# Kernel tuning notes

Hardware: AMD Instinct MI355X
Metric: run time of the kernel (lower is better)

The kernel has to match this reference:

```python
import jax, jax.numpy as jnp
import numpy as np

N = 100000   # nodes
F = 128      # input features
H = 128      # hidden = 2*output_dim
Z = 64       # output_dim
E = 1600000  # message-passing edges
EP = 200000  # pos/neg decode edges each


def setup_inputs() -> dict:
    key = jax.random.key(0)
    ks = jax.random.split(key, 6)
    x = jax.random.normal(ks[0], (N, F), dtype=jnp.float32)
    edge_index = jax.random.randint(ks[1], (2, E), 0, N, dtype=jnp.int64)
    pos_edge = jax.random.randint(ks[2], (2, EP), 0, N, dtype=jnp.int64)
    neg_edge = jax.random.randint(ks[3], (2, EP), 0, N, dtype=jnp.int64)
    W1 = jax.random.normal(ks[4], (F, H), dtype=jnp.float32) / np.float32(np.sqrt(F))
    b1 = jnp.zeros((H,), jnp.float32)
    W2 = jax.random.normal(ks[5], (H, Z), dtype=jnp.float32) / np.float32(np.sqrt(H))
    b2 = jnp.zeros((Z,), jnp.float32)
    return dict(x=x, W1=W1, b1=b1, W2=W2, b2=b2,
                edge_index=edge_index, pos_edge=pos_edge, neg_edge=neg_edge)


def _gcn_conv(x, src, dst, norm, W, b, n):
    # x' = scatter_add_dst(norm * (x @ W)[src]) + b   (GCNConv, sym-normalized, self-loops)
    h = x @ W                         # [N, out]
    msg = h[src] * norm[:, None]      # [E+N, out] gather + scale
    out = jax.ops.segment_sum(msg, dst, num_segments=n)
    return out + b


def reference(x, W1, b1, W2, b2, edge_index, pos_edge, neg_edge):
    # add self-loops (GCNConv default)
    loop = jnp.arange(N, dtype=edge_index.dtype)
    src = jnp.concatenate([edge_index[0], loop])
    dst = jnp.concatenate([edge_index[1], loop])
    # symmetric normalization deg^-1/2[src] * deg^-1/2[dst]
    deg = jax.ops.segment_sum(jnp.ones(dst.shape, x.dtype), dst, num_segments=N)
    dinv = jnp.where(deg > 0, jax.lax.rsqrt(deg), 0.0)
    norm = dinv[src] * dinv[dst]
    # encoder: GCN -> ReLU -> GCN
    h = jax.nn.relu(_gcn_conv(x, src, dst, norm, W1, b1, N))
    latent = _gcn_conv(h, src, dst, norm, W2, b2, N)
    # decoder: edge dot products on pos+neg edges
    e = jnp.concatenate([pos_edge, neg_edge], axis=-1)  # [2, 2*EP]
    logits = jnp.sum(latent[e[0]] * latent[e[1]], axis=-1)
    return logits
```

## Files before the change

### kernel.cpp

```cpp
#include <hip/hip_runtime.h>

#define N_NODES 100000
#define F_IN    128
#define H_DIM   128
#define Z_DIM   64
#define E_EDGES 1600000
#define EP_EDGES 200000

#define BSHIFT 7
#define NBUCK  ((N_NODES + 127) >> 7)
#define CHUNK  4096
#define NCHUNK ((E_EDGES + CHUNK - 1) / CHUNK)

typedef __attribute__((ext_vector_type(8))) short short8;
typedef __attribute__((ext_vector_type(4))) float f32x4;
typedef unsigned int uint;
typedef unsigned short ushort;

__device__ __forceinline__ ushort f2bf(float f) {
    uint u = __float_as_uint(f);
    u += 0x7fffu + ((u >> 16) & 1u);
    return (ushort)(u >> 16);
}
__device__ __forceinline__ float bflo(uint u) { return __uint_as_float(u << 16); }
__device__ __forceinline__ float bfhi(uint u) { return __uint_as_float(u & 0xffff0000u); }


__global__ __launch_bounds__(256) void wprep_kernel(const float* __restrict__ W1,
                                                    const float* __restrict__ W2,
                                                    ushort* __restrict__ W1T,
                                                    ushort* __restrict__ W2T,
                                                    int* __restrict__ gcur) {
    int i = blockIdx.x * 256 + threadIdx.x;
    if (i < 1024) gcur[i] = 0;
    if (i < 128 * 128) {
        int n = i >> 7, k = i & 127;
        W1T[i] = f2bf(W1[k * 128 + n]);
    }
    int j = i - 128 * 128;
    if (j >= 0 && j < 64 * 128) {
        int n = j >> 7, k = j & 127;
        W2T[j] = f2bf(W2[k * 64 + n]);
    }
}


__global__ __launch_bounds__(256) void bhist_kernel(const int* __restrict__ dst,
                                                    int* __restrict__ gcur,
                                                    int* __restrict__ tbl) {
    __shared__ int lh[NBUCK];
    for (int i = threadIdx.x; i < NBUCK; i += 256) lh[i] = 0;
    __syncthreads();
    int base = blockIdx.x * CHUNK;
    int end = min(base + CHUNK, E_EDGES);
    for (int e = base + threadIdx.x; e < end; e += 256)
        atomicAdd(&lh[dst[e] >> BSHIFT], 1);
    __syncthreads();
    int* trow = tbl + (size_t)blockIdx.x * NBUCK;
    for (int i = threadIdx.x; i < NBUCK; i += 256) {
        int c = lh[i];
        trow[i] = c;
        if (c) atomicAdd(&gcur[i], c);
    }
}


__global__ __launch_bounds__(1024) void bscan_kernel(int* __restrict__ gc) {
    __shared__ int s[1024];
    int t = threadIdx.x;
    int v = (t < NBUCK) ? gc[t] : 0;
    s[t] = v;
    __syncthreads();
    #pragma unroll
    for (int off = 1; off < 1024; off <<= 1) {
        int x = (t >= off) ? s[t - off] : 0;
        __syncthreads();
        s[t] += x;
        __syncthreads();
    }
    if (t < NBUCK) gc[t] = s[t] - v;
}


__global__ __launch_bounds__(512) void chunk_scan_kernel(int* __restrict__ tbl,
                                                         const int* __restrict__ gcur) {
    __shared__ int s[512];
    int b = blockIdx.x, t = threadIdx.x;
    int v = (t < NCHUNK) ? tbl[(size_t)t * NBUCK + b] : 0;
    s[t] = v;
    __syncthreads();
    #pragma unroll
    for (int off = 1; off < 512; off <<= 1) {
        int x = (t >= off) ? s[t - off] : 0;
        __syncthreads();
        s[t] += x;
        __syncthreads();
    }
    if (t < NCHUNK)
        tbl[(size_t)t * NBUCK + b] = gcur[b] + (s[t] - v);
}


__global__ __launch_bounds__(256) void bscatter_kernel(const int* __restrict__ src,
                                                       const int* __restrict__ dst,
                                                       const int* __restrict__ tbl,
                                                       int* __restrict__ sorted) {
    __shared__ int lbase[NBUCK];
    int c = blockIdx.x;
    const int* trow = tbl + (size_t)c * NBUCK;
    for (int i = threadIdx.x; i < NBUCK; i += 256) lbase[i] = trow[i];
    __syncthreads();
    int base = c * CHUNK;
    int end = min(base + CHUNK, E_EDGES);
    for (int e = base + threadIdx.x; e < end; e += 256) {
        int d = dst[e];
        int p = atomicAdd(&lbase[d >> BSHIFT], 1);
        sorted[p] = (src[e] << 7) | (d & 127);
    }
}


__global__ __launch_bounds__(256) void bucket_csr_kernel(const int* __restrict__ sorted,
                                                         const int* __restrict__ gcur,
                                                         int* __restrict__ csr,
                                                         int* __restrict__ ends,
                                                         float* __restrict__ dinv) {
    __shared__ int lcnt[4][128], lcur[4][128];
    int b = blockIdx.x, t = threadIdx.x;
    int wave = t >> 6;
    int bstart = gcur[b];
    int bend = (b + 1 < NBUCK) ? gcur[b + 1] : E_EDGES;
    if (t < 128) { lcnt[0][t] = 0; lcnt[1][t] = 0; }
    else { int u = t - 128; lcnt[2][u] = 0; lcnt[3][u] = 0; }
    __syncthreads();
    for (int i = bstart + t; i < bend; i += 256)
        atomicAdd(&lcnt[wave][sorted[i] & 127], 1);
    __syncthreads();
    if (t < 64) {
        int w0a = lcnt[0][t], w1a = lcnt[1][t], w2a = lcnt[2][t], w3a = lcnt[3][t];
        int w0b = lcnt[0][t + 64], w1b = lcnt[1][t + 64], w2b = lcnt[2][t + 64], w3b = lcnt[3][t + 64];
        int c0 = w0a + w1a + w2a + w3a;
        int c1 = w0b + w1b + w2b + w3b;
        int s0 = c0;
        #pragma unroll
        for (int d = 1; d < 64; d <<= 1) {
            int x = __shfl_up(s0, d, 64);
            if (t >= d) s0 += x;
        }
        int tot0 = __shfl(s0, 63, 64);
        int s1 = c1;
        #pragma unroll
        for (int d = 1; d < 64; d <<= 1) {
            int x = __shfl_up(s1, d, 64);
            if (t >= d) s1 += x;
        }
        s1 += tot0;
        int basea = bstart + s0 - c0;
        int baseb = bstart + s1 - c1;
        lcur[0][t] = basea;
        lcur[1][t] = basea + w0a;
        lcur[2][t] = basea + w0a + w1a;
        lcur[3][t] = basea + w0a + w1a + w2a;
        lcur[0][t + 64] = baseb;
        lcur[1][t + 64] = baseb + w0b;
        lcur[2][t + 64] = baseb + w0b + w1b;
        lcur[3][t + 64] = baseb + w0b + w1b + w2b;
        int n0 = b * 128 + t, n1 = n0 + 64;
        if (n0 < N_NODES) { ends[n0] = bstart + s0; dinv[n0] = rsqrtf(1.0f + (float)c0); }
        if (n1 < N_NODES) { ends[n1] = bstart + s1; dinv[n1] = rsqrtf(1.0f + (float)c1); }
    }
    __syncthreads();
    for (int i = bstart + t; i < bend; i += 256) {
        int v = sorted[i];
        int p = atomicAdd(&lcur[wave][v & 127], 1);
        csr[p] = v >> 7;
    }
}


template<int NC, bool A_F32>
__global__ __launch_bounds__(256) void gemm_mfma_kernel(const void* __restrict__ Ap,
                                                        const ushort* __restrict__ BT,
                                                        const float* __restrict__ dinv,
                                                        ushort* __restrict__ C, int M) {
    constexpr int NT = NC / 16;
    __shared__ ushort Bs[4 * NT * 64 * 8];

    for (int idx = threadIdx.x; idx < 4 * NT * 64; idx += 256) {
        int l   = idx & 63;
        int nt  = (idx >> 6) % NT;
        int kc  = idx / (64 * NT);
        int m16 = l & 15, quad = l >> 4;
        ((short8*)Bs)[idx] =
            *(const short8*)(BT + ((nt * 16 + m16) * 128 + kc * 32 + quad * 8));
    }
    __syncthreads();

    int wave = threadIdx.x >> 6, lane = threadIdx.x & 63;
    int m16 = lane & 15, quad = lane >> 4;
    int row0 = (blockIdx.x * 4 + wave) * 16;
    if (row0 >= M) return;
    int arow = row0 + m16;
    if (arow >= M) arow = M - 1;

    f32x4 acc[NT];
    #pragma unroll
    for (int t = 0; t < NT; ++t) acc[t] = (f32x4){0.f, 0.f, 0.f, 0.f};

    #pragma unroll
    for (int kc = 0; kc < 4; ++kc) {
        short8 a;
        if (A_F32) {
            const float* A = (const float*)Ap;
            const float4* p = (const float4*)(A + (size_t)arow * 128 + kc * 32 + quad * 8);
            float4 x0 = p[0], x1 = p[1];
            a[0] = (short)f2bf(x0.x); a[1] = (short)f2bf(x0.y);
            a[2] = (short)f2bf(x0.z); a[3] = (short)f2bf(x0.w);
            a[4] = (short)f2bf(x1.x); a[5] = (short)f2bf(x1.y);
            a[6] = (short)f2bf(x1.z); a[7] = (short)f2bf(x1.w);
        } else {
            a = *(const short8*)((const ushort*)Ap + (size_t)arow * 128 + kc * 32 + quad * 8);
        }
        #pragma unroll
        for (int nt = 0; nt < NT; ++nt) {
            short8 b = ((const short8*)Bs)[(kc * NT + nt) * 64 + lane];
            acc[nt] = __builtin_amdgcn_mfma_f32_16x16x32_bf16(a, b, acc[nt], 0, 0, 0);
        }
    }

    #pragma unroll
    for (int r = 0; r < 4; ++r) {
        int row = row0 + quad * 4 + r;
        if (row < M) {
            float dr = dinv[row];
            #pragma unroll
            for (int nt = 0; nt < NT; ++nt)
                C[(size_t)row * NC + nt * 16 + m16] = f2bf(acc[nt][r] * dr);
        }
    }
}


__global__ __launch_bounds__(256) void gather128_kernel(const ushort* __restrict__ feat,
                                                        const float* __restrict__ bias,
                                                        const float* __restrict__ dinv,
                                                        const int* __restrict__ ends,
                                                        const int* __restrict__ csr,
                                                        ushort* __restrict__ out) {
    int wave = threadIdx.x >> 6, lane = threadIdx.x & 63;
    int half = lane >> 5, sl = lane & 31;
    int n = blockIdx.x * 4 + wave;
    const uint2* fu = (const uint2*)feat;

    float a0 = 0.f, a1 = 0.f, a2 = 0.f, a3 = 0.f;
    if (half == 0) {
        uint2 s = fu[(size_t)n * 32 + sl];
        a0 = bflo(s.x); a1 = bfhi(s.x); a2 = bflo(s.y); a3 = bfhi(s.y);
    }
    int j0 = n ? ends[n - 1] : 0, j1 = ends[n];
    int j = j0 + half;
    for (; j + 14 < j1; j += 16) {
        int s0 = csr[j],      s1 = csr[j + 2],  s2 = csr[j + 4],  s3 = csr[j + 6];
        int s4 = csr[j + 8],  s5 = csr[j + 10], s6 = csr[j + 12], s7 = csr[j + 14];
        uint2 f0 = fu[(size_t)s0 * 32 + sl];
        uint2 f1 = fu[(size_t)s1 * 32 + sl];
        uint2 f2 = fu[(size_t)s2 * 32 + sl];
        uint2 f3 = fu[(size_t)s3 * 32 + sl];
        uint2 f4 = fu[(size_t)s4 * 32 + sl];
        uint2 f5 = fu[(size_t)s5 * 32 + sl];
        uint2 f6 = fu[(size_t)s6 * 32 + sl];
        uint2 f7 = fu[(size_t)s7 * 32 + sl];
        a0 += bflo(f0.x) + bflo(f1.x) + bflo(f2.x) + bflo(f3.x)
            + bflo(f4.x) + bflo(f5.x) + bflo(f6.x) + bflo(f7.x);
        a1 += bfhi(f0.x) + bfhi(f1.x) + bfhi(f2.x) + bfhi(f3.x)
            + bfhi(f4.x) + bfhi(f5.x) + bfhi(f6.x) + bfhi(f7.x);
        a2 += bflo(f0.y) + bflo(f1.y) + bflo(f2.y) + bflo(f3.y)
            + bflo(f4.y) + bflo(f5.y) + bflo(f6.y) + bflo(f7.y);
        a3 += bfhi(f0.y) + bfhi(f1.y) + bfhi(f2.y) + bfhi(f3.y)
            + bfhi(f4.y) + bfhi(f5.y) + bfhi(f6.y) + bfhi(f7.y);
    }
    for (; j + 6 < j1; j += 8) {
        int s0 = csr[j], s1 = csr[j + 2], s2 = csr[j + 4], s3 = csr[j + 6];
        uint2 f0 = fu[(size_t)s0 * 32 + sl];
        uint2 f1 = fu[(size_t)s1 * 32 + sl];
        uint2 f2 = fu[(size_t)s2 * 32 + sl];
        uint2 f3 = fu[(size_t)s3 * 32 + sl];
        a0 += bflo(f0.x) + bflo(f1.x) + bflo(f2.x) + bflo(f3.x);
        a1 += bfhi(f0.x) + bfhi(f1.x) + bfhi(f2.x) + bfhi(f3.x);
        a2 += bflo(f0.y) + bflo(f1.y) + bflo(f2.y) + bflo(f3.y);
        a3 += bfhi(f0.y) + bfhi(f1.y) + bfhi(f2.y) + bfhi(f3.y);
    }
    for (; j < j1; j += 2) {
        uint2 f = fu[(size_t)csr[j] * 32 + sl];
        a0 += bflo(f.x); a1 += bfhi(f.x); a2 += bflo(f.y); a3 += bfhi(f.y);
    }
    a0 += __shfl_xor(a0, 32, 64);
    a1 += __shfl_xor(a1, 32, 64);
    a2 += __shfl_xor(a2, 32, 64);
    a3 += __shfl_xor(a3, 32, 64);
    if (half == 0) {
        float dn = dinv[n];
        float r0 = fmaxf(bias[sl * 4 + 0] + dn * a0, 0.f);
        float r1 = fmaxf(bias[sl * 4 + 1] + dn * a1, 0.f);
        float r2 = fmaxf(bias[sl * 4 + 2] + dn * a2, 0.f);
        float r3 = fmaxf(bias[sl * 4 + 3] + dn * a3, 0.f);
        uint2 o;
        o.x = (uint)f2bf(r0) | ((uint)f2bf(r1) << 16);
        o.y = (uint)f2bf(r2) | ((uint)f2bf(r3) << 16);
        ((uint2*)out)[(size_t)n * 32 + sl] = o;
    }
}


__global__ __launch_bounds__(256) void gather64_kernel(const ushort* __restrict__ feat,
                                                       const float* __restrict__ bias,
                                                       const float* __restrict__ dinv,
                                                       const int* __restrict__ ends,
                                                       const int* __restrict__ csr,
                                                       ushort* __restrict__ outB) {
    int wave = threadIdx.x >> 6, lane = threadIdx.x & 63;
    int half = lane >> 5, sl = lane & 31;
    int n = blockIdx.x * 4 + wave;
    const uint* fu = (const uint*)feat;

    float a0 = 0.f, a1 = 0.f;
    if (half == 0) {
        uint s = fu[(size_t)n * 32 + sl];
        a0 = bflo(s); a1 = bfhi(s);
    }
    int j0 = n ? ends[n - 1] : 0, j1 = ends[n];
    int j = j0 + half;
    for (; j + 14 < j1; j += 16) {
        int s0 = csr[j],      s1 = csr[j + 2],  s2 = csr[j + 4],  s3 = csr[j + 6];
        int s4 = csr[j + 8],  s5 = csr[j + 10], s6 = csr[j + 12], s7 = csr[j + 14];
        uint f0 = fu[(size_t)s0 * 32 + sl];
        uint f1 = fu[(size_t)s1 * 32 + sl];
        uint f2 = fu[(size_t)s2 * 32 + sl];
        uint f3 = fu[(size_t)s3 * 32 + sl];
        uint f4 = fu[(size_t)s4 * 32 + sl];
        uint f5 = fu[(size_t)s5 * 32 + sl];
        uint f6 = fu[(size_t)s6 * 32 + sl];
        uint f7 = fu[(size_t)s7 * 32 + sl];
        a0 += bflo(f0) + bflo(f1) + bflo(f2) + bflo(f3)
            + bflo(f4) + bflo(f5) + bflo(f6) + bflo(f7);
        a1 += bfhi(f0) + bfhi(f1) + bfhi(f2) + bfhi(f3)
            + bfhi(f4) + bfhi(f5) + bfhi(f6) + bfhi(f7);
    }
    for (; j + 6 < j1; j += 8) {
        int s0 = csr[j], s1 = csr[j + 2], s2 = csr[j + 4], s3 = csr[j + 6];
        uint f0 = fu[(size_t)s0 * 32 + sl];
        uint f1 = fu[(size_t)s1 * 32 + sl];
        uint f2 = fu[(size_t)s2 * 32 + sl];
        uint f3 = fu[(size_t)s3 * 32 + sl];
        a0 += bflo(f0) + bflo(f1) + bflo(f2) + bflo(f3);
        a1 += bfhi(f0) + bfhi(f1) + bfhi(f2) + bfhi(f3);
    }
    for (; j < j1; j += 2) {
        uint f = fu[(size_t)csr[j] * 32 + sl];
        a0 += bflo(f); a1 += bfhi(f);
    }
    a0 += __shfl_xor(a0, 32, 64);
    a1 += __shfl_xor(a1, 32, 64);
    if (half == 0) {
        float dn = dinv[n];
        float o0 = bias[sl * 2]     + dn * a0;
        float o1 = bias[sl * 2 + 1] + dn * a1;
        ((uint*)outB)[(size_t)n * 32 + sl] = (uint)f2bf(o0) | ((uint)f2bf(o1) << 16);
    }
}


__global__ __launch_bounds__(256) void decode_kernel(const ushort* __restrict__ latentB,
                                                     const int* __restrict__ pos,
                                                     const int* __restrict__ neg,
                                                     float* __restrict__ out) {
    int gwave = (blockIdx.x * 256 + threadIdx.x) >> 6;
    int lane = threadIdx.x & 63;
    int half = lane >> 5, sl = lane & 31;
    const uint* L = (const uint*)latentB;
    int e0 = gwave * 8 + half * 4;
    if (e0 >= 2 * EP_EDGES) return;

    int ia[4], ib[4];
    #pragma unroll
    for (int u = 0; u < 4; ++u) {
        int edge = e0 + u;
        if (edge < EP_EDGES) {
            ia[u] = pos[edge];
            ib[u] = pos[EP_EDGES + edge];
        } else {
            int e2 = edge - EP_EDGES;
            ia[u] = neg[e2];
            ib[u] = neg[EP_EDGES + e2];
        }
    }
    uint la[4], lb[4];
    #pragma unroll
    for (int u = 0; u < 4; ++u) {
        la[u] = L[(size_t)ia[u] * 32 + sl];
        lb[u] = L[(size_t)ib[u] * 32 + sl];
    }
    float v[4];
    #pragma unroll
    for (int u = 0; u < 4; ++u)
        v[u] = bflo(la[u]) * bflo(lb[u]) + bfhi(la[u]) * bfhi(lb[u]);
    #pragma unroll
    for (int u = 0; u < 4; ++u) {
        float s = v[u];
        #pragma unroll
        for (int off = 16; off > 0; off >>= 1) s += __shfl_down(s, off, 64);
        if (sl == 0) out[e0 + u] = s;
    }
}


extern "C" void kernel_launch(void* const* d_in, const int* in_sizes, int n_in,
                              void* d_out, int out_size, void* d_ws, size_t ws_size,
                              hipStream_t stream) {
    const float* x  = (const float*)d_in[0];
    const float* W1 = (const float*)d_in[1];
    const float* b1 = (const float*)d_in[2];
    const float* W2 = (const float*)d_in[3];
    const float* b2 = (const float*)d_in[4];
    const int* edge_index = (const int*)d_in[5];
    const int* pos = (const int*)d_in[6];
    const int* neg = (const int*)d_in[7];
    float* out = (float*)d_out;

    const int* src = edge_index;
    const int* dst = edge_index + E_EDGES;

    float*  dinv   = (float*)d_ws;
    int*    ends   = (int*)(dinv + N_NODES);
    int*    gcur   = ends + N_NODES;
    int*    tbl    = gcur + 1024;
    int*    sorted = tbl + NCHUNK * NBUCK;
    int*    csr    = sorted + E_EDGES;
    ushort* W1T    = (ushort*)(csr + E_EDGES);
    ushort* W2T    = W1T + 128 * 128;
    ushort* bufH   = (ushort*)(((uintptr_t)(W2T + 64 * 128) + 255) & ~(uintptr_t)255);
    ushort* bufR   = bufH + (size_t)N_NODES * 128;

    wprep_kernel<<<96, 256, 0, stream>>>(W1, W2, W1T, W2T, gcur);

    bhist_kernel<<<NCHUNK, 256, 0, stream>>>(dst, gcur, tbl);
    bscan_kernel<<<1, 1024, 0, stream>>>(gcur);
    chunk_scan_kernel<<<NBUCK, 512, 0, stream>>>(tbl, gcur);
    bscatter_kernel<<<NCHUNK, 256, 0, stream>>>(src, dst, tbl, sorted);
    bucket_csr_kernel<<<NBUCK, 256, 0, stream>>>(sorted, gcur, csr, ends, dinv);

    const int GEMM_GRID = (N_NODES + 63) / 64;

    gemm_mfma_kernel<128, true><<<GEMM_GRID, 256, 0, stream>>>(x, W1T, dinv, bufH, N_NODES);

    gather128_kernel<<<N_NODES / 4, 256, 0, stream>>>(bufH, b1, dinv, ends, csr, bufR);

    gemm_mfma_kernel<64, false><<<GEMM_GRID, 256, 0, stream>>>(bufR, W2T, dinv, bufH, N_NODES);

    ushort* latentB = bufR;
    gather64_kernel<<<N_NODES / 4, 256, 0, stream>>>(bufH, b2, dinv, ends, csr, latentB);

    decode_kernel<<<(2 * EP_EDGES) / 32, 256, 0, stream>>>(latentB, pos, neg, out);
}
```

Measured before the change: 318.7 us.

## Restructure CSR gather kernels with 16-byte loads and shuffled index broadcast

Both SpMM gather kernels now split each wave into 4 (128-dim) or 8 (64-dim) lane groups. Each lane issues 16-byte feature loads, and each group handles a different neighbor. Neighbor indices are loaded once per 64-edge batch with a coalesced read and broadcast through wave shuffles, instead of each lane re-reading csr. This aims to raise memory-level parallelism and cut index-load traffic, at the cost of more cross-lane reductions and masked tail handling. Launch bounds also request 8 blocks per CU.

```diff
diff --git a/kernel.cpp b/kernel.cpp
--- a/kernel.cpp
+++ b/kernel.cpp
@@ -241,131 +241,184 @@
 }
 
 
-__global__ __launch_bounds__(256) void gather128_kernel(const ushort* __restrict__ feat,
-                                                        const float* __restrict__ bias,
-                                                        const float* __restrict__ dinv,
-                                                        const int* __restrict__ ends,
-                                                        const int* __restrict__ csr,
-                                                        ushort* __restrict__ out) {
+__global__ __launch_bounds__(256, 8) void gather128_kernel(const ushort* __restrict__ feat,
+                                                           const float* __restrict__ bias,
+                                                           const float* __restrict__ dinv,
+                                                           const int* __restrict__ ends,
+                                                           const int* __restrict__ csr,
+                                                           ushort* __restrict__ out) {
     int wave = threadIdx.x >> 6, lane = threadIdx.x & 63;
-    int half = lane >> 5, sl = lane & 31;
+    int q = lane >> 4, ql = lane & 15;
     int n = blockIdx.x * 4 + wave;
-    const uint2* fu = (const uint2*)feat;
+    const uint4* F = (const uint4*)feat;
 
     float a0 = 0.f, a1 = 0.f, a2 = 0.f, a3 = 0.f;
-    if (half == 0) {
-        uint2 s = fu[(size_t)n * 32 + sl];
+    float a4 = 0.f, a5 = 0.f, a6 = 0.f, a7 = 0.f;
+    if (q == 0) {
+        uint4 s = F[(uint)n * 16u + (uint)ql];
         a0 = bflo(s.x); a1 = bfhi(s.x); a2 = bflo(s.y); a3 = bfhi(s.y);
+        a4 = bflo(s.z); a5 = bfhi(s.z); a6 = bflo(s.w); a7 = bfhi(s.w);
     }
     int j0 = n ? ends[n - 1] : 0, j1 = ends[n];
-    int j = j0 + half;
-    for (; j + 14 < j1; j += 16) {
-        int s0 = csr[j],      s1 = csr[j + 2],  s2 = csr[j + 4],  s3 = csr[j + 6];
-        int s4 = csr[j + 8],  s5 = csr[j + 10], s6 = csr[j + 12], s7 = csr[j + 14];
-        uint2 f0 = fu[(size_t)s0 * 32 + sl];
-        uint2 f1 = fu[(size_t)s1 * 32 + sl];
-        uint2 f2 = fu[(size_t)s2 * 32 + sl];
-        uint2 f3 = fu[(size_t)s3 * 32 + sl];
-        uint2 f4 = fu[(size_t)s4 * 32 + sl];
-        uint2 f5 = fu[(size_t)s5 * 32 + sl];
-        uint2 f6 = fu[(size_t)s6 * 32 + sl];
-        uint2 f7 = fu[(size_t)s7 * 32 + sl];
-        a0 += bflo(f0.x) + bflo(f1.x) + bflo(f2.x) + bflo(f3.x)
-            + bflo(f4.x) + bflo(f5.x) + bflo(f6.x) + bflo(f7.x);
-        a1 += bfhi(f0.x) + bfhi(f1.x) + bfhi(f2.x) + bfhi(f3.x)
-            + bfhi(f4.x) + bfhi(f5.x) + bfhi(f6.x) + bfhi(f7.x);
-        a2 += bflo(f0.y) + bflo(f1.y) + bflo(f2.y) + bflo(f3.y)
-            + bflo(f4.y) + bflo(f5.y) + bflo(f6.y) + bflo(f7.y);
-        a3 += bfhi(f0.y) + bfhi(f1.y) + bfhi(f2.y) + bfhi(f3.y)
-            + bfhi(f4.y) + bfhi(f5.y) + bfhi(f6.y) + bfhi(f7.y);
-    }
-    for (; j + 6 < j1; j += 8) {
-        int s0 = csr[j], s1 = csr[j + 2], s2 = csr[j + 4], s3 = csr[j + 6];
-        uint2 f0 = fu[(size_t)s0 * 32 + sl];
-        uint2 f1 = fu[(size_t)s1 * 32 + sl];
-        uint2 f2 = fu[(size_t)s2 * 32 + sl];
-        uint2 f3 = fu[(size_t)s3 * 32 + sl];
-        a0 += bflo(f0.x) + bflo(f1.x) + bflo(f2.x) + bflo(f3.x);
-        a1 += bfhi(f0.x) + bfhi(f1.x) + bfhi(f2.x) + bfhi(f3.x);
-        a2 += bflo(f0.y) + bflo(f1.y) + bflo(f2.y) + bflo(f3.y);
-        a3 += bfhi(f0.y) + bfhi(f1.y) + bfhi(f2.y) + bfhi(f3.y);
-    }
-    for (; j < j1; j += 2) {
-        uint2 f = fu[(size_t)csr[j] * 32 + sl];
-        a0 += bflo(f.x); a1 += bfhi(f.x); a2 += bflo(f.y); a3 += bfhi(f.y);
-    }
-    a0 += __shfl_xor(a0, 32, 64);
-    a1 += __shfl_xor(a1, 32, 64);
-    a2 += __shfl_xor(a2, 32, 64);
-    a3 += __shfl_xor(a3, 32, 64);
-    if (half == 0) {
+    for (int base = j0; base < j1; base += 64) {
+        int m = min(64, j1 - base);
+        int idxv = csr[base + min(lane, m - 1)];
+        int nch = m >> 4;
+        for (int c = 0; c < nch; ++c) {
+            int e = c * 16 + q;
+            int s0 = __shfl(idxv, e, 64);
+            int s1 = __shfl(idxv, e + 4, 64);
+            int s2 = __shfl(idxv, e + 8, 64);
+            int s3 = __shfl(idxv, e + 12, 64);
+            uint4 r0 = F[(uint)s0 * 16u + (uint)ql];
+            uint4 r1 = F[(uint)s1 * 16u + (uint)ql];
+            uint4 r2 = F[(uint)s2 * 16u + (uint)ql];
+            uint4 r3 = F[(uint)s3 * 16u + (uint)ql];
+            a0 += bflo(r0.x) + bflo(r1.x) + bflo(r2.x) + bflo(r3.x);
+            a1 += bfhi(r0.x) + bfhi(r1.x) + bfhi(r2.x) + bfhi(r3.x);
+            a2 += bflo(r0.y) + bflo(r1.y) + bflo(r2.y) + bflo(r3.y);
+            a3 += bfhi(r0.y) + bfhi(r1.y) + bfhi(r2.y) + bfhi(r3.y);
+            a4 += bflo(r0.z) + bflo(r1.z) + bflo(r2.z) + bflo(r3.z);
+            a5 += bfhi(r0.z) + bfhi(r1.z) + bfhi(r2.z) + bfhi(r3.z);
+            a6 += bflo(r0.w) + bflo(r1.w) + bflo(r2.w) + bflo(r3.w);
+            a7 += bfhi(r0.w) + bfhi(r1.w) + bfhi(r2.w) + bfhi(r3.w);
+        }
+        if (nch * 16 < m) {
+            int e = nch * 16 + q;
+            int mc = m - 1;
+            int t0 = __shfl(idxv, min(e,      mc), 64);
+            int t1 = __shfl(idxv, min(e + 4,  mc), 64);
+            int t2 = __shfl(idxv, min(e + 8,  mc), 64);
+            int t3 = __shfl(idxv, min(e + 12, mc), 64);
+            uint4 r0 = F[(uint)t0 * 16u + (uint)ql];
+            uint4 r1 = F[(uint)t1 * 16u + (uint)ql];
+            uint4 r2 = F[(uint)t2 * 16u + (uint)ql];
+            uint4 r3 = F[(uint)t3 * 16u + (uint)ql];
+            if (e < m) {
+                a0 += bflo(r0.x); a1 += bfhi(r0.x); a2 += bflo(r0.y); a3 += bfhi(r0.y);
+                a4 += bflo(r0.z); a5 += bfhi(r0.z); a6 += bflo(r0.w); a7 += bfhi(r0.w);
+            }
+            if (e + 4 < m) {
+                a0 += bflo(r1.x); a1 += bfhi(r1.x); a2 += bflo(r1.y); a3 += bfhi(r1.y);
+                a4 += bflo(r1.z); a5 += bfhi(r1.z); a6 += bflo(r1.w); a7 += bfhi(r1.w);
+            }
+            if (e + 8 < m) {
+                a0 += bflo(r2.x); a1 += bfhi(r2.x); a2 += bflo(r2.y); a3 += bfhi(r2.y);
+                a4 += bflo(r2.z); a5 += bfhi(r2.z); a6 += bflo(r2.w); a7 += bfhi(r2.w);
+            }
+            if (e + 12 < m) {
+                a0 += bflo(r3.x); a1 += bfhi(r3.x); a2 += bflo(r3.y); a3 += bfhi(r3.y);
+                a4 += bflo(r3.z); a5 += bfhi(r3.z); a6 += bflo(r3.w); a7 += bfhi(r3.w);
+            }
+        }
+    }
+    a0 += __shfl_xor(a0, 16, 64); a0 += __shfl_xor(a0, 32, 64);
+    a1 += __shfl_xor(a1, 16, 64); a1 += __shfl_xor(a1, 32, 64);
+    a2 += __shfl_xor(a2, 16, 64); a2 += __shfl_xor(a2, 32, 64);
+    a3 += __shfl_xor(a3, 16, 64); a3 += __shfl_xor(a3, 32, 64);
+    a4 += __shfl_xor(a4, 16, 64); a4 += __shfl_xor(a4, 32, 64);
+    a5 += __shfl_xor(a5, 16, 64); a5 += __shfl_xor(a5, 32, 64);
+    a6 += __shfl_xor(a6, 16, 64); a6 += __shfl_xor(a6, 32, 64);
+    a7 += __shfl_xor(a7, 16, 64); a7 += __shfl_xor(a7, 32, 64);
+    if (q == 0) {
         float dn = dinv[n];
-        float r0 = fmaxf(bias[sl * 4 + 0] + dn * a0, 0.f);
-        float r1 = fmaxf(bias[sl * 4 + 1] + dn * a1, 0.f);
-        float r2 = fmaxf(bias[sl * 4 + 2] + dn * a2, 0.f);
-        float r3 = fmaxf(bias[sl * 4 + 3] + dn * a3, 0.f);
-        uint2 o;
+        const float4* bp = (const float4*)(bias + ql * 8);
+        float4 b0 = bp[0], b1v = bp[1];
+        float r0 = fmaxf(b0.x + dn * a0, 0.f);
+        float r1 = fmaxf(b0.y + dn * a1, 0.f);
+        float r2 = fmaxf(b0.z + dn * a2, 0.f);
+        float r3 = fmaxf(b0.w + dn * a3, 0.f);
+        float r4 = fmaxf(b1v.x + dn * a4, 0.f);
+        float r5 = fmaxf(b1v.y + dn * a5, 0.f);
+        float r6 = fmaxf(b1v.z + dn * a6, 0.f);
+        float r7 = fmaxf(b1v.w + dn * a7, 0.f);
+        uint4 o;
         o.x = (uint)f2bf(r0) | ((uint)f2bf(r1) << 16);
         o.y = (uint)f2bf(r2) | ((uint)f2bf(r3) << 16);
-        ((uint2*)out)[(size_t)n * 32 + sl] = o;
-    }
-}
-
-
-__global__ __launch_bounds__(256) void gather64_kernel(const ushort* __restrict__ feat,
-                                                       const float* __restrict__ bias,
-                                                       const float* __restrict__ dinv,
-                                                       const int* __restrict__ ends,
-                                                       const int* __restrict__ csr,
-                                                       ushort* __restrict__ outB) {
+        o.z = (uint)f2bf(r4) | ((uint)f2bf(r5) << 16);
+        o.w = (uint)f2bf(r6) | ((uint)f2bf(r7) << 16);
+        ((uint4*)out)[(uint)n * 16u + (uint)ql] = o;
+    }
+}
+
+
+__global__ __launch_bounds__(256, 8) void gather64_kernel(const ushort* __restrict__ feat,
+                                                          const float* __restrict__ bias,
+                                                          const float* __restrict__ dinv,
+                                                          const int* __restrict__ ends,
+                                                          const int* __restrict__ csr,
+                                                          ushort* __restrict__ outB) {
     int wave = threadIdx.x >> 6, lane = threadIdx.x & 63;
-    int half = lane >> 5, sl = lane & 31;
+    int g = lane >> 3, gl = lane & 7;
     int n = blockIdx.x * 4 + wave;
-    const uint* fu = (const uint*)feat;
-
-    float a0 = 0.f, a1 = 0.f;
-    if (half == 0) {
-        uint s = fu[(size_t)n * 32 + sl];
-        a0 = bflo(s); a1 = bfhi(s);
+    const uint4* F = (const uint4*)feat;
+
+    float a0 = 0.f, a1 = 0.f, a2 = 0.f, a3 = 0.f;
+    float a4 = 0.f, a5 = 0.f, a6 = 0.f, a7 = 0.f;
+    if (g == 0) {
+        uint4 s = F[(uint)n * 8u + (uint)gl];
+        a0 = bflo(s.x); a1 = bfhi(s.x); a2 = bflo(s.y); a3 = bfhi(s.y);
+        a4 = bflo(s.z); a5 = bfhi(s.z); a6 = bflo(s.w); a7 = bfhi(s.w);
     }
     int j0 = n ? ends[n - 1] : 0, j1 = ends[n];
-    int j = j0 + half;
-    for (; j + 14 < j1; j += 16) {
-        int s0 = csr[j],      s1 = csr[j + 2],  s2 = csr[j + 4],  s3 = csr[j + 6];
-        int s4 = csr[j + 8],  s5 = csr[j + 10], s6 = csr[j + 12], s7 = csr[j + 14];
-        uint f0 = fu[(size_t)s0 * 32 + sl];
-        uint f1 = fu[(size_t)s1 * 32 + sl];
-        uint f2 = fu[(size_t)s2 * 32 + sl];
-        uint f3 = fu[(size_t)s3 * 32 + sl];
-        uint f4 = fu[(size_t)s4 * 32 + sl];
-        uint f5 = fu[(size_t)s5 * 32 + sl];
-        uint f6 = fu[(size_t)s6 * 32 + sl];
-        uint f7 = fu[(size_t)s7 * 32 + sl];
-        a0 += bflo(f0) + bflo(f1) + bflo(f2) + bflo(f3)
-            + bflo(f4) + bflo(f5) + bflo(f6) + bflo(f7);
-        a1 += bfhi(f0) + bfhi(f1) + bfhi(f2) + bfhi(f3)
-            + bfhi(f4) + bfhi(f5) + bfhi(f6) + bfhi(f7);
-    }
-    for (; j + 6 < j1; j += 8) {
-        int s0 = csr[j], s1 = csr[j + 2], s2 = csr[j + 4], s3 = csr[j + 6];
-        uint f0 = fu[(size_t)s0 * 32 + sl];
-        uint f1 = fu[(size_t)s1 * 32 + sl];
-        uint f2 = fu[(size_t)s2 * 32 + sl];
-        uint f3 = fu[(size_t)s3 * 32 + sl];
-        a0 += bflo(f0) + bflo(f1) + bflo(f2) + bflo(f3);
-        a1 += bfhi(f0) + bfhi(f1) + bfhi(f2) + bfhi(f3);
-    }
-    for (; j < j1; j += 2) {
-        uint f = fu[(size_t)csr[j] * 32 + sl];
-        a0 += bflo(f); a1 += bfhi(f);
-    }
-    a0 += __shfl_xor(a0, 32, 64);
-    a1 += __shfl_xor(a1, 32, 64);
-    if (half == 0) {
+    for (int base = j0; base < j1; base += 64) {
+        int m = min(64, j1 - base);
+        int idxv = csr[base + min(lane, m - 1)];
+        int nch = m >> 4;
+        for (int c = 0; c < nch; ++c) {
+            int e = c * 16 + g;
+            int s0 = __shfl(idxv, e, 64);
+            int s1 = __shfl(idxv, e + 8, 64);
+            uint4 r0 = F[(uint)s0 * 8u + (uint)gl];
+            uint4 r1 = F[(uint)s1 * 8u + (uint)gl];
+            a0 += bflo(r0.x) + bflo(r1.x); a1 += bfhi(r0.x) + bfhi(r1.x);
+            a2 += bflo(r0.y) + bflo(r1.y); a3 += bfhi(r0.y) + bfhi(r1.y);
+            a4 += bflo(r0.z) + bflo(r1.z); a5 += bfhi(r0.z) + bfhi(r1.z);
+            a6 += bflo(r0.w) + bflo(r1.w); a7 += bfhi(r0.w) + bfhi(r1.w);
+        }
+        if (nch * 16 < m) {
+            int e = nch * 16 + g;
+            int mc = m - 1;
+            int t0 = __shfl(idxv, min(e,     mc), 64);
+            int t1 = __shfl(idxv, min(e + 8, mc), 64);
+            uint4 r0 = F[(uint)t0 * 8u + (uint)gl];
+            uint4 r1 = F[(uint)t1 * 8u + (uint)gl];
+            if (e < m) {
+                a0 += bflo(r0.x); a1 += bfhi(r0.x); a2 += bflo(r0.y); a3 += bfhi(r0.y);
+                a4 += bflo(r0.z); a5 += bfhi(r0.z); a6 += bflo(r0.w); a7 += bfhi(r0.w);
+            }
+            if (e + 8 < m) {
+                a0 += bflo(r1.x); a1 += bfhi(r1.x); a2 += bflo(r1.y); a3 += bfhi(r1.y);
+                a4 += bflo(r1.z); a5 += bfhi(r1.z); a6 += bflo(r1.w); a7 += bfhi(r1.w);
+            }
+        }
+    }
+    a0 += __shfl_xor(a0, 8, 64); a0 += __shfl_xor(a0, 16, 64); a0 += __shfl_xor(a0, 32, 64);
+    a1 += __shfl_xor(a1, 8, 64); a1 += __shfl_xor(a1, 16, 64); a1 += __shfl_xor(a1, 32, 64);
+    a2 += __shfl_xor(a2, 8, 64); a2 += __shfl_xor(a2, 16, 64); a2 += __shfl_xor(a2, 32, 64);
+    a3 += __shfl_xor(a3, 8, 64); a3 += __shfl_xor(a3, 16, 64); a3 += __shfl_xor(a3, 32, 64);
+    a4 += __shfl_xor(a4, 8, 64); a4 += __shfl_xor(a4, 16, 64); a4 += __shfl_xor(a4, 32, 64);
+    a5 += __shfl_xor(a5, 8, 64); a5 += __shfl_xor(a5, 16, 64); a5 += __shfl_xor(a5, 32, 64);
+    a6 += __shfl_xor(a6, 8, 64); a6 += __shfl_xor(a6, 16, 64); a6 += __shfl_xor(a6, 32, 64);
+    a7 += __shfl_xor(a7, 8, 64); a7 += __shfl_xor(a7, 16, 64); a7 += __shfl_xor(a7, 32, 64);
+    if (g == 0) {
         float dn = dinv[n];
-        float o0 = bias[sl * 2]     + dn * a0;
-        float o1 = bias[sl * 2 + 1] + dn * a1;
-        ((uint*)outB)[(size_t)n * 32 + sl] = (uint)f2bf(o0) | ((uint)f2bf(o1) << 16);
+        const float4* bp = (const float4*)(bias + gl * 8);
+        float4 b0 = bp[0], b1v = bp[1];
+        float r0 = b0.x + dn * a0;
+        float r1 = b0.y + dn * a1;
+        float r2 = b0.z + dn * a2;
+        float r3 = b0.w + dn * a3;
+        float r4 = b1v.x + dn * a4;
+        float r5 = b1v.y + dn * a5;
+        float r6 = b1v.z + dn * a6;
+        float r7 = b1v.w + dn * a7;
+        uint4 o;
+        o.x = (uint)f2bf(r0) | ((uint)f2bf(r1) << 16);
+        o.y = (uint)f2bf(r2) | ((uint)f2bf(r3) << 16);
+        o.z = (uint)f2bf(r4) | ((uint)f2bf(r5) << 16);
+        o.w = (uint)f2bf(r6) | ((uint)f2bf(r7) << 16);
+        ((uint4*)outB)[(uint)n * 8u + (uint)gl] = o;
     }
 }
 
```

New measurement: 312.2 us. -2.1%, faster.

## Restructure CSR gathers as full-wave rows with readlane-broadcast neighbour indices

Applied to the files above, without the earlier changes.

Both aggregation kernels now use the whole 64-lane wave for one destination row instead of two half-waves that each handle alternate edges. Neighbour indices are loaded coalesced, 64 per chunk, and broadcast with readlane, so the per-edge feature addresses are wave-uniform and the scattered scalar index loads go away. Two accumulators split the dependency chain, and launch_bounds gets an occupancy hint of 8. In exchange each feature load is narrower (4 or 2 bytes per lane), so fewer bytes are in flight per instruction, which could hurt latency hiding on the random gathers.

```diff
diff --git a/kernel.cpp b/kernel.cpp
--- a/kernel.cpp
+++ b/kernel.cpp
@@ -241,132 +241,121 @@
 }
 
 
-__global__ __launch_bounds__(256) void gather128_kernel(const ushort* __restrict__ feat,
-                                                        const float* __restrict__ bias,
-                                                        const float* __restrict__ dinv,
-                                                        const int* __restrict__ ends,
-                                                        const int* __restrict__ csr,
-                                                        ushort* __restrict__ out) {
+__global__ __launch_bounds__(256, 8) void gather128_kernel(const ushort* __restrict__ feat,
+                                                           const float* __restrict__ bias,
+                                                           const float* __restrict__ dinv,
+                                                           const int* __restrict__ ends,
+                                                           const int* __restrict__ csr,
+                                                           ushort* __restrict__ out) {
     int wave = threadIdx.x >> 6, lane = threadIdx.x & 63;
-    int half = lane >> 5, sl = lane & 31;
     int n = blockIdx.x * 4 + wave;
-    const uint2* fu = (const uint2*)feat;
-
-    float a0 = 0.f, a1 = 0.f, a2 = 0.f, a3 = 0.f;
-    if (half == 0) {
-        uint2 s = fu[(size_t)n * 32 + sl];
-        a0 = bflo(s.x); a1 = bfhi(s.x); a2 = bflo(s.y); a3 = bfhi(s.y);
-    }
+    const uint* F = (const uint*)feat;
+    uint rowoff = (uint)n * 64u + (uint)lane;
+
+    uint su = F[rowoff];
+    float l0 = bflo(su), h0 = bfhi(su);
+    float l1 = 0.f, h1 = 0.f;
+
     int j0 = n ? ends[n - 1] : 0, j1 = ends[n];
-    int j = j0 + half;
-    for (; j + 14 < j1; j += 16) {
-        int s0 = csr[j],      s1 = csr[j + 2],  s2 = csr[j + 4],  s3 = csr[j + 6];
-        int s4 = csr[j + 8],  s5 = csr[j + 10], s6 = csr[j + 12], s7 = csr[j + 14];
-        uint2 f0 = fu[(size_t)s0 * 32 + sl];
-        uint2 f1 = fu[(size_t)s1 * 32 + sl];
-        uint2 f2 = fu[(size_t)s2 * 32 + sl];
-        uint2 f3 = fu[(size_t)s3 * 32 + sl];
-        uint2 f4 = fu[(size_t)s4 * 32 + sl];
-        uint2 f5 = fu[(size_t)s5 * 32 + sl];
-        uint2 f6 = fu[(size_t)s6 * 32 + sl];
-        uint2 f7 = fu[(size_t)s7 * 32 + sl];
-        a0 += bflo(f0.x) + bflo(f1.x) + bflo(f2.x) + bflo(f3.x)
-            + bflo(f4.x) + bflo(f5.x) + bflo(f6.x) + bflo(f7.x);
-        a1 += bfhi(f0.x) + bfhi(f1.x) + bfhi(f2.x) + bfhi(f3.x)
-            + bfhi(f4.x) + bfhi(f5.x) + bfhi(f6.x) + bfhi(f7.x);
-        a2 += bflo(f0.y) + bflo(f1.y) + bflo(f2.y) + bflo(f3.y)
-            + bflo(f4.y) + bflo(f5.y) + bflo(f6.y) + bflo(f7.y);
-        a3 += bfhi(f0.y) + bfhi(f1.y) + bfhi(f2.y) + bfhi(f3.y)
-            + bfhi(f4.y) + bfhi(f5.y) + bfhi(f6.y) + bfhi(f7.y);
-    }
-    for (; j + 6 < j1; j += 8) {
-        int s0 = csr[j], s1 = csr[j + 2], s2 = csr[j + 4], s3 = csr[j + 6];
-        uint2 f0 = fu[(size_t)s0 * 32 + sl];
-        uint2 f1 = fu[(size_t)s1 * 32 + sl];
-        uint2 f2 = fu[(size_t)s2 * 32 + sl];
-        uint2 f3 = fu[(size_t)s3 * 32 + sl];
-        a0 += bflo(f0.x) + bflo(f1.x) + bflo(f2.x) + bflo(f3.x);
-        a1 += bfhi(f0.x) + bfhi(f1.x) + bfhi(f2.x) + bfhi(f3.x);
-        a2 += bflo(f0.y) + bflo(f1.y) + bflo(f2.y) + bflo(f3.y);
-        a3 += bfhi(f0.y) + bfhi(f1.y) + bfhi(f2.y) + bfhi(f3.y);
-    }
-    for (; j < j1; j += 2) {
-        uint2 f = fu[(size_t)csr[j] * 32 + sl];
-        a0 += bflo(f.x); a1 += bfhi(f.x); a2 += bflo(f.y); a3 += bfhi(f.y);
-    }
-    a0 += __shfl_xor(a0, 32, 64);
-    a1 += __shfl_xor(a1, 32, 64);
-    a2 += __shfl_xor(a2, 32, 64);
-    a3 += __shfl_xor(a3, 32, 64);
-    if (half == 0) {
-        float dn = dinv[n];
-        float r0 = fmaxf(bias[sl * 4 + 0] + dn * a0, 0.f);
-        float r1 = fmaxf(bias[sl * 4 + 1] + dn * a1, 0.f);
-        float r2 = fmaxf(bias[sl * 4 + 2] + dn * a2, 0.f);
-        float r3 = fmaxf(bias[sl * 4 + 3] + dn * a3, 0.f);
-        uint2 o;
-        o.x = (uint)f2bf(r0) | ((uint)f2bf(r1) << 16);
-        o.y = (uint)f2bf(r2) | ((uint)f2bf(r3) << 16);
-        ((uint2*)out)[(size_t)n * 32 + sl] = o;
-    }
-}
-
-
-__global__ __launch_bounds__(256) void gather64_kernel(const ushort* __restrict__ feat,
-                                                       const float* __restrict__ bias,
-                                                       const float* __restrict__ dinv,
-                                                       const int* __restrict__ ends,
-                                                       const int* __restrict__ csr,
-                                                       ushort* __restrict__ outB) {
+    j0 = __builtin_amdgcn_readfirstlane(j0);
+    j1 = __builtin_amdgcn_readfirstlane(j1);
+
+    for (int base = j0; base < j1; base += 64) {
+        int m = min(64, j1 - base);
+        int idxv = csr[base + min(lane, m - 1)];
+        int e = 0;
+        for (; e + 8 <= m; e += 8) {
+            int s0 = __builtin_amdgcn_readlane(idxv, e + 0);
+            int s1 = __builtin_amdgcn_readlane(idxv, e + 1);
+            int s2 = __builtin_amdgcn_readlane(idxv, e + 2);
+            int s3 = __builtin_amdgcn_readlane(idxv, e + 3);
+            int s4 = __builtin_amdgcn_readlane(idxv, e + 4);
+            int s5 = __builtin_amdgcn_readlane(idxv, e + 5);
+            int s6 = __builtin_amdgcn_readlane(idxv, e + 6);
+            int s7 = __builtin_amdgcn_readlane(idxv, e + 7);
+            uint r0 = F[(uint)s0 * 64u + (uint)lane];
+            uint r1 = F[(uint)s1 * 64u + (uint)lane];
+            uint r2 = F[(uint)s2 * 64u + (uint)lane];
+            uint r3 = F[(uint)s3 * 64u + (uint)lane];
+            uint r4 = F[(uint)s4 * 64u + (uint)lane];
+            uint r5 = F[(uint)s5 * 64u + (uint)lane];
+            uint r6 = F[(uint)s6 * 64u + (uint)lane];
+            uint r7 = F[(uint)s7 * 64u + (uint)lane];
+            l0 += bflo(r0) + bflo(r2);
+            l1 += bflo(r1) + bflo(r3);
+            h0 += bfhi(r0) + bfhi(r2);
+            h1 += bfhi(r1) + bfhi(r3);
+            l0 += bflo(r4) + bflo(r6);
+            l1 += bflo(r5) + bflo(r7);
+            h0 += bfhi(r4) + bfhi(r6);
+            h1 += bfhi(r5) + bfhi(r7);
+        }
+        for (; e < m; ++e) {
+            int s = __builtin_amdgcn_readlane(idxv, e);
+            uint r = F[(uint)s * 64u + (uint)lane];
+            l0 += bflo(r); h0 += bfhi(r);
+        }
+    }
+    float dn = dinv[n];
+    float2 bv = ((const float2*)bias)[lane];
+    float rlo = fmaxf(bv.x + dn * (l0 + l1), 0.f);
+    float rhi = fmaxf(bv.y + dn * (h0 + h1), 0.f);
+    ((uint*)out)[rowoff] = (uint)f2bf(rlo) | ((uint)f2bf(rhi) << 16);
+}
+
+
+__global__ __launch_bounds__(256, 8) void gather64_kernel(const ushort* __restrict__ feat,
+                                                          const float* __restrict__ bias,
+                                                          const float* __restrict__ dinv,
+                                                          const int* __restrict__ ends,
+                                                          const int* __restrict__ csr,
+                                                          ushort* __restrict__ outB) {
     int wave = threadIdx.x >> 6, lane = threadIdx.x & 63;
-    int half = lane >> 5, sl = lane & 31;
     int n = blockIdx.x * 4 + wave;
-    const uint* fu = (const uint*)feat;
-
-    float a0 = 0.f, a1 = 0.f;
-    if (half == 0) {
-        uint s = fu[(size_t)n * 32 + sl];
-        a0 = bflo(s); a1 = bfhi(s);
-    }
+    uint rowoff = (uint)n * 64u + (uint)lane;
+
+    float a0 = __uint_as_float((uint)feat[rowoff] << 16);
+    float a1 = 0.f;
+
     int j0 = n ? ends[n - 1] : 0, j1 = ends[n];
-    int j = j0 + half;
-    for (; j + 14 < j1; j += 16) {
-        int s0 = csr[j],      s1 = csr[j + 2],  s2 = csr[j + 4],  s3 = csr[j + 6];
-        int s4 = csr[j + 8],  s5 = csr[j + 10], s6 = csr[j + 12], s7 = csr[j + 14];
-        uint f0 = fu[(size_t)s0 * 32 + sl];
-        uint f1 = fu[(size_t)s1 * 32 + sl];
-        uint f2 = fu[(size_t)s2 * 32 + sl];
-        uint f3 = fu[(size_t)s3 * 32 + sl];
-        uint f4 = fu[(size_t)s4 * 32 + sl];
-        uint f5 = fu[(size_t)s5 * 32 + sl];
-        uint f6 = fu[(size_t)s6 * 32 + sl];
-        uint f7 = fu[(size_t)s7 * 32 + sl];
-        a0 += bflo(f0) + bflo(f1) + bflo(f2) + bflo(f3)
-            + bflo(f4) + bflo(f5) + bflo(f6) + bflo(f7);
-        a1 += bfhi(f0) + bfhi(f1) + bfhi(f2) + bfhi(f3)
-            + bfhi(f4) + bfhi(f5) + bfhi(f6) + bfhi(f7);
-    }
-    for (; j + 6 < j1; j += 8) {
-        int s0 = csr[j], s1 = csr[j + 2], s2 = csr[j + 4], s3 = csr[j + 6];
-        uint f0 = fu[(size_t)s0 * 32 + sl];
-        uint f1 = fu[(size_t)s1 * 32 + sl];
-        uint f2 = fu[(size_t)s2 * 32 + sl];
-        uint f3 = fu[(size_t)s3 * 32 + sl];
-        a0 += bflo(f0) + bflo(f1) + bflo(f2) + bflo(f3);
-        a1 += bfhi(f0) + bfhi(f1) + bfhi(f2) + bfhi(f3);
-    }
-    for (; j < j1; j += 2) {
-        uint f = fu[(size_t)csr[j] * 32 + sl];
-        a0 += bflo(f); a1 += bfhi(f);
-    }
-    a0 += __shfl_xor(a0, 32, 64);
-    a1 += __shfl_xor(a1, 32, 64);
-    if (half == 0) {
-        float dn = dinv[n];
-        float o0 = bias[sl * 2]     + dn * a0;
-        float o1 = bias[sl * 2 + 1] + dn * a1;
-        ((uint*)outB)[(size_t)n * 32 + sl] = (uint)f2bf(o0) | ((uint)f2bf(o1) << 16);
-    }
+    j0 = __builtin_amdgcn_readfirstlane(j0);
+    j1 = __builtin_amdgcn_readfirstlane(j1);
+
+    for (int base = j0; base < j1; base += 64) {
+        int m = min(64, j1 - base);
+        int idxv = csr[base + min(lane, m - 1)];
+        int e = 0;
+        for (; e + 8 <= m; e += 8) {
+            int s0 = __builtin_amdgcn_readlane(idxv, e + 0);
+            int s1 = __builtin_amdgcn_readlane(idxv, e + 1);
+            int s2 = __builtin_amdgcn_readlane(idxv, e + 2);
+            int s3 = __builtin_amdgcn_readlane(idxv, e + 3);
+            int s4 = __builtin_amdgcn_readlane(idxv, e + 4);
+            int s5 = __builtin_amdgcn_readlane(idxv, e + 5);
+            int s6 = __builtin_amdgcn_readlane(idxv, e + 6);
+            int s7 = __builtin_amdgcn_readlane(idxv, e + 7);
+            uint r0 = feat[(uint)s0 * 64u + (uint)lane];
+            uint r1 = feat[(uint)s1 * 64u + (uint)lane];
+            uint r2 = feat[(uint)s2 * 64u + (uint)lane];
+            uint r3 = feat[(uint)s3 * 64u + (uint)lane];
+            uint r4 = feat[(uint)s4 * 64u + (uint)lane];
+            uint r5 = feat[(uint)s5 * 64u + (uint)lane];
+            uint r6 = feat[(uint)s6 * 64u + (uint)lane];
+            uint r7 = feat[(uint)s7 * 64u + (uint)lane];
+            a0 += __uint_as_float(r0 << 16) + __uint_as_float(r2 << 16);
+            a1 += __uint_as_float(r1 << 16) + __uint_as_float(r3 << 16);
+            a0 += __uint_as_float(r4 << 16) + __uint_as_float(r6 << 16);
+            a1 += __uint_as_float(r5 << 16) + __uint_as_float(r7 << 16);
+        }
+        for (; e < m; ++e) {
+            int s = __builtin_amdgcn_readlane(idxv, e);
+            uint r = feat[(uint)s * 64u + (uint)lane];
+            a0 += __uint_as_float(r << 16);
+        }
+    }
+    float dn = dinv[n];
+    float o = bias[lane] + dn * (a0 + a1);
+    outB[rowoff] = f2bf(o);
 }
 
 
```

New measurement: 320.0 us. Within noise of the previous version (+0.4%).
